# Optimization experiments

Hardware: AMD Instinct MI355X
Metric: run time of the kernel (lower is better)

The kernel has to match this reference:

```python
import jax, jax.numpy as jnp
import numpy as np

B, T, C, H, N = 2, 1024, 2048, 32, 64  # C == H*N, head_size fixed at 64
LAYER, NLAYERS = 12, 24
EPS = 1e-5 * 64.0  # GroupNorm eps = 1e-5 * 8**2


def _structured_params():
    r01 = LAYER / (NLAYERS - 1)          # ratio_0_to_1
    r1a0 = 1.0 - LAYER / NLAYERS         # ratio_1_to_almost0
    ddd = np.arange(C, dtype=np.float64) / C
    n = np.arange(C, dtype=np.float64)
    p = {}
    p['maa_x'] = 1.0 - ddd ** r1a0
    p['maa_w'] = 1.0 - ddd ** r1a0
    p['maa_k'] = 1.0 - ddd ** r1a0
    p['maa_v'] = 1.0 - (ddd ** r1a0 + 0.3 * r01)
    p['maa_r'] = 1.0 - ddd ** (0.5 * r1a0)
    p['maa_g'] = 1.0 - ddd ** (0.5 * r1a0)
    p['time_decay'] = -6.0 + 5.0 * (n / (C - 1)) ** (0.7 + 1.3 * r01)
    zig = ((n + 1) % 3 - 1) * 0.1
    p['u'] = (r01 * (1.0 - n / (C - 1)) + zig).reshape(H, N)  # time_faaaa
    return {k: jnp.asarray(v, jnp.float32) for k, v in p.items()}


def setup_inputs():
    key = jax.random.key(0)
    ks = jax.random.split(key, 12)
    inp = {'x': jax.random.normal(ks[0], (B, T, C), jnp.float32)}
    inp.update(_structured_params())
    inp['maa_w1'] = jax.random.uniform(ks[1], (C, 5 * 32), jnp.float32, -1e-4, 1e-4)
    inp['maa_w2'] = jax.random.uniform(ks[2], (5, 32, C), jnp.float32, -1e-4, 1e-4)
    inp['td_w1'] = jax.random.uniform(ks[3], (C, 64), jnp.float32, -1e-4, 1e-4)
    inp['td_w2'] = jax.random.uniform(ks[4], (64, C), jnp.float32, -1e-4, 1e-4)
    for i, name in enumerate(['Wr', 'Wk', 'Wv', 'Wg', 'Wo']):
        inp[name] = jax.random.normal(ks[5 + i], (C, C), jnp.float32) * 0.02  # applied as x @ W
    inp['ln_g'] = jnp.ones((C,), jnp.float32)
    inp['ln_b'] = jnp.zeros((C,), jnp.float32)
    return inp


def _wkv6(r, k, v, w, u):
    # r,k,v,w: [B,T,C]; u: [H,N].  y_t = r_t . (u*k_t v_t^T + S_t); S_{t+1} = exp(-exp(w_t))*S_t + k_t v_t^T
    def heads(a):
        return a.reshape(B, T, H, N).transpose(1, 0, 2, 3)  # [T,B,H,N]
    r, k, v = heads(r), heads(k), heads(v)
    d = jnp.exp(-jnp.exp(heads(w)))  # data-dependent per-channel decay

    def step(S, inp):
        r_t, k_t, v_t, d_t = inp  # each [B,H,N]
        y = jnp.einsum('bhj,bhji->bhi', r_t, S) \
            + jnp.sum(r_t * u * k_t, axis=-1, keepdims=True) * v_t
        S = d_t[..., None] * S + k_t[..., None] * v_t[..., None, :]
        return S, y

    S0 = jnp.zeros((B, H, N, N), jnp.float32)
    _, y = jax.lax.scan(step, S0, (r, k, v, d))
    return y.transpose(1, 0, 2, 3).reshape(B, T, C)


def reference(x, maa_x, maa_w, maa_k, maa_v, maa_r, maa_g, time_decay, u,
              maa_w1, maa_w2, td_w1, td_w2, Wr, Wk, Wv, Wg, Wo, ln_g, ln_b):
    # token shift: ZeroPad2d((0,0,1,-1)) == shift right by one along T with zero at t=0
    xx = jnp.pad(x, ((0, 0), (1, 0), (0, 0)))[:, :-1] - x
    xxx = x + xx * maa_x
    m = jnp.tanh(xxx @ maa_w1).reshape(B, T, 5, 32)
    m = jnp.einsum('btfd,fdc->fbtc', m, maa_w2)  # [5,B,T,C]
    mw, mk, mv, mr, mg = m[0], m[1], m[2], m[3], m[4]
    xw = x + xx * (maa_w + mw)
    xk = x + xx * (maa_k + mk)
    xv = x + xx * (maa_v + mv)
    xr = x + xx * (maa_r + mr)
    xg = x + xx * (maa_g + mg)
    r = xr @ Wr
    k = xk @ Wk
    v = xv @ Wv
    g = jax.nn.silu(xg @ Wg)
    w = time_decay + jnp.tanh(xw @ td_w1) @ td_w2  # [B,T,C]

    y = _wkv6(r, k, v, w, u)

    # GroupNorm(H groups over C), applied per (b,t) row
    yh = y.reshape(B, T, H, N)
    mu = yh.mean(-1, keepdims=True)
    var = yh.var(-1, keepdims=True)
    yn = (yh - mu) * jax.lax.rsqrt(var + EPS)
    yn = yn * ln_g.reshape(H, N) + ln_b.reshape(H, N)
    y = yn.reshape(B, T, C)
    return (y * g) @ Wo
```

## Files before the change

### kernel.cpp

```cpp
#include <hip/hip_runtime.h>
#include <cstdint>
#include <cstddef>

#define B_  2
#define T_  1024
#define C_  2048
#define H_  32
#define BT_ (B_*T_)
static constexpr float EPS_GN = 1e-5f * 64.0f;

using short8 = __attribute__((ext_vector_type(8))) short;
using f32x4  = __attribute__((ext_vector_type(4))) float;
typedef unsigned short bfu16;

__device__ __forceinline__ bfu16 f2b(float f) {
  uint32_t x = __float_as_uint(f);
  uint32_t r = (x + 0x7FFFu + ((x >> 16) & 1u)) >> 16;
  return (bfu16)r;
}
__device__ __forceinline__ float b2f(bfu16 h) {
  return __uint_as_float(((uint32_t)h) << 16);
}

__device__ __forceinline__ void gload16(const bfu16* g, bfu16* l) {
  __builtin_amdgcn_global_load_lds((__attribute__((address_space(1))) void*)g,
                                   (__attribute__((address_space(3))) void*)l,
                                   16, 0, 0);
}

struct G256P {
  const bfu16* Bt; float* of;
  size_t bStr, oStr;
  int ldk, nkt, kSplit;
  const bfu16* aArr[4];
};

__global__ __launch_bounds__(512, 2)
void gemm256(G256P p)
{
  extern __shared__ __align__(16) bfu16 sm[];
  const int tid  = threadIdx.x;
  const int z    = blockIdx.z;
  const int m0   = blockIdx.y * 256, n0 = blockIdx.x * 256;
  const int lane = tid & 63;
  const int wv   = tid >> 6;
  const int wm   = wv >> 2, wn = wv & 3;
  const int ldk  = p.ldk;

  const bfu16* A;
  size_t koff;
  if (p.kSplit > 1) { A = p.aArr[0]; koff = (size_t)z * p.nkt * 64; }
  else             { A = p.aArr[z]; koff = 0; }
  const bfu16* Bt = p.Bt + (size_t)z * p.bStr;

  const int srow = tid >> 3;
  const int scol = (tid & 7) * 8;
  const int sswz = (srow & 7) << 3;
  const bfu16* gA = A  + (size_t)(m0 + srow) * ldk + koff + (scol ^ sswz);
  const bfu16* gB = Bt + (size_t)(n0 + srow) * ldk + koff + (scol ^ sswz);

  auto STAGE_A = [&](bfu16* dst, int kt) {
    const bfu16* g = gA + (size_t)kt * 64;
    bfu16* l = dst + srow * 64 + scol;
#pragma unroll
    for (int it = 0; it < 4; ++it)
      gload16(g + (size_t)it * 64 * ldk, l + it * 4096);
  };
  auto STAGE_B = [&](bfu16* dst, int kt) {
    const bfu16* g = gB + (size_t)kt * 64;
    bfu16* l = dst + srow * 64 + scol;
#pragma unroll
    for (int it = 0; it < 4; ++it)
      gload16(g + (size_t)it * 64 * ldk, l + it * 4096);
  };

  f32x4 acc[8][4];
  const f32x4 zero = {0.f, 0.f, 0.f, 0.f};
#pragma unroll
  for (int i = 0; i < 8; ++i)
#pragma unroll
    for (int j = 0; j < 4; ++j) acc[i][j] = zero;

  STAGE_A(sm, 0);
  STAGE_B(sm + 32768, 0);

  const int rswz = (lane & 7) << 3;

  for (int kt = 0; kt < p.nkt; ++kt) {
    bfu16* curA = sm + (kt & 1) * 16384;
    bfu16* curB = sm + 32768 + (kt & 1) * 16384;
    bfu16* nxtA = sm + ((kt & 1) ^ 1) * 16384;
    bfu16* nxtB = sm + 32768 + ((kt & 1) ^ 1) * 16384;
    const bool more = (kt + 1 < p.nkt);
    if (more) {
      STAGE_A(nxtA, kt + 1);
      asm volatile("s_waitcnt vmcnt(4)" ::: "memory");
    } else {
      asm volatile("s_waitcnt vmcnt(0)" ::: "memory");
    }
    __builtin_amdgcn_s_barrier();

#pragma unroll
    for (int ks = 0; ks < 2; ++ks) {
      if (ks == 1 && more) STAGE_B(nxtB, kt + 1);
      const int ko = (ks * 32 + (lane >> 4) * 8) ^ rswz;
      short8 a[8], b[4];
#pragma unroll
      for (int i = 0; i < 8; ++i)
        a[i] = *(const short8*)(curA + (wm * 128 + i * 16 + (lane & 15)) * 64 + ko);
#pragma unroll
      for (int j = 0; j < 4; ++j)
        b[j] = *(const short8*)(curB + (wn * 64 + j * 16 + (lane & 15)) * 64 + ko);
      __builtin_amdgcn_s_setprio(1);
#pragma unroll
      for (int i = 0; i < 8; ++i)
#pragma unroll
        for (int j = 0; j < 4; ++j)
          acc[i][j] = __builtin_amdgcn_mfma_f32_16x16x32_bf16(a[i], b[j], acc[i][j], 0, 0, 0);
      __builtin_amdgcn_s_setprio(0);
    }
    __builtin_amdgcn_s_barrier();
  }

  float* o = p.of + (size_t)z * p.oStr;
  const int cb = n0 + wn * 64 + (lane & 15);
  const int rb = m0 + wm * 128 + ((lane >> 4) << 2);
#pragma unroll
  for (int i = 0; i < 8; ++i)
#pragma unroll
    for (int j = 0; j < 4; ++j) {
      int col = cb + j * 16;
#pragma unroll
      for (int q = 0; q < 4; ++q)
        o[(size_t)(rb + i * 16 + q) * 2048 + col] = acc[i][j][q];
    }
}

struct GemmP {
  const bfu16* A; const bfu16* Bt;
  float* of; bfu16* ob;
  const bfu16* xh; const bfu16* xxh;
  int ldk, kIters, kChunk, ldo;
  size_t pStride, aStr, bStr, oStr;
  const float* vArr[5];
};

template<int MODE>
__global__ __launch_bounds__(256)
void gemm_k(GemmP p)
{
  __shared__ alignas(16) bfu16 As[128*64];
  __shared__ alignas(16) bfu16 Bs[128*64];
  const int tid  = threadIdx.x;
  const int z    = blockIdx.z;
  const int m0   = blockIdx.y * 128, n0 = blockIdx.x * 128;
  const int lane = tid & 63;
  const int wv   = tid >> 6;
  const int wr   = (wv >> 1) * 64, wc = (wv & 1) * 64;

  const bfu16* A  = p.A;
  const bfu16* Bt = p.Bt;
  size_t koff = 0;
  if constexpr (MODE == 7) { A += (size_t)z * p.aStr; Bt += (size_t)z * p.bStr; }
  if constexpr (MODE == 5) { koff = (size_t)z * p.kChunk; }

  f32x4 acc[4][4];
  const f32x4 zero = {0.f, 0.f, 0.f, 0.f};
#pragma unroll
  for (int i = 0; i < 4; ++i)
#pragma unroll
    for (int j = 0; j < 4; ++j) acc[i][j] = zero;

  const int srow = tid >> 3;
  const int scol = (tid & 7) * 8;
  const int ldk  = p.ldk;

  for (int kb = 0; kb < p.kIters; ++kb) {
    const bfu16* ga = A  + (size_t)m0 * ldk + koff + kb * 64;
    const bfu16* gb = Bt + (size_t)n0 * ldk + koff + kb * 64;
#pragma unroll
    for (int it = 0; it < 4; ++it) {
      int r = it * 32 + srow;
      gload16(ga + (size_t)r * ldk + scol, As + r * 64 + scol);
      gload16(gb + (size_t)r * ldk + scol, Bs + r * 64 + scol);
    }
    __syncthreads();
#pragma unroll
    for (int kk = 0; kk < 2; ++kk) {
      const int ko = kk * 32 + (lane >> 4) * 8;
      short8 a[4], b[4];
#pragma unroll
      for (int i = 0; i < 4; ++i)
        a[i] = *(const short8*)(As + (wr + i * 16 + (lane & 15)) * 64 + ko);
#pragma unroll
      for (int j = 0; j < 4; ++j)
        b[j] = *(const short8*)(Bs + (wc + j * 16 + (lane & 15)) * 64 + ko);
#pragma unroll
      for (int i = 0; i < 4; ++i)
#pragma unroll
        for (int j = 0; j < 4; ++j)
          acc[i][j] = __builtin_amdgcn_mfma_f32_16x16x32_bf16(a[i], b[j], acc[i][j], 0, 0, 0);
    }
    __syncthreads();
  }

  const int cb = n0 + wc + (lane & 15);
  const int rb = m0 + wr + ((lane >> 4) << 2);
#pragma unroll
  for (int i = 0; i < 4; ++i) {
#pragma unroll
    for (int j = 0; j < 4; ++j) {
      int col = cb + j * 16;
#pragma unroll
      for (int q = 0; q < 4; ++q) {
        int row = rb + i * 16 + q;
        float v = acc[i][j][q];
        if constexpr (MODE == 4) {
          p.of[(size_t)row * p.ldo + col] = p.vArr[0][col] + v;
        } else if constexpr (MODE == 5) {
          p.of[(size_t)z * p.pStride + (size_t)row * p.ldo + col] = v;
        } else if constexpr (MODE == 7) {
          size_t idx = (size_t)row * C_ + col;
          (p.ob + (size_t)z * p.oStr)[idx] =
              f2b(b2f(p.xh[idx]) + b2f(p.xxh[idx]) * (p.vArr[z][col] + v));
        }
      }
    }
  }
}

template<int OUT>
__global__ __launch_bounds__(256)
void redk_tanh(const float* __restrict__ part, size_t pStr, int ldo, int ncols,
               bfu16* __restrict__ out)
{
  int id = blockIdx.x * 256 + threadIdx.x;
  int row = id / ncols, col = id % ncols;
  if (row >= BT_) return;
  float v = 0.f;
#pragma unroll
  for (int s = 0; s < 8; ++s) v += part[(size_t)s * pStr + (size_t)row * ldo + col];
  bfu16 tv = f2b(tanhf(v));
  if constexpr (OUT == 0)
    out[((size_t)(col >> 5) * BT_ + row) * 64 + (col & 31)] = tv;
  else
    out[(size_t)row * 64 + col] = tv;
}

__global__ __launch_bounds__(256)
void redk_sum2(const float* __restrict__ p0, float* __restrict__ out)
{
  size_t i = ((size_t)blockIdx.x * 256 + threadIdx.x) * 4;
  float4 a = *(const float4*)(p0 + i);
  float4 b = *(const float4*)(p0 + (size_t)2048 * 2048 + i);
  a.x += b.x; a.y += b.y; a.z += b.z; a.w += b.w;
  *(float4*)(out + i) = a;
}

struct TrP { const float* src[5]; bfu16* dst; size_t dStr; int R, Cc, Rpad, ldd; };

__global__ __launch_bounds__(256)
void transpose_k(TrP p)
{
  __shared__ float tile[32][33];
  const float* src = p.src[blockIdx.z];
  bfu16* dst = p.dst + (size_t)blockIdx.z * p.dStr;
  const int tx = threadIdx.x & 31, ty = threadIdx.x >> 5;
  const int r0 = blockIdx.y * 32, c0 = blockIdx.x * 32;
#pragma unroll
  for (int i = 0; i < 4; ++i) {
    int r = r0 + ty + i * 8, c = c0 + tx;
    tile[ty + i * 8][tx] = (r < p.R && c < p.Cc) ? src[(size_t)r * p.Cc + c] : 0.f;
  }
  __syncthreads();
#pragma unroll
  for (int i = 0; i < 4; ++i) {
    int c = c0 + ty + i * 8, r = r0 + tx;
    if (c < p.Cc && r < p.Rpad) dst[(size_t)c * p.ldd + r] = f2b(tile[tx][ty + i * 8]);
  }
}

__global__ __launch_bounds__(256)
void prep_xx(const float* __restrict__ x, const float* __restrict__ maa_x,
             bfu16* __restrict__ xxh, bfu16* __restrict__ xxx,
             bfu16* __restrict__ xh)
{
  size_t i = ((size_t)blockIdx.x * 256 + threadIdx.x) * 4;
  int c  = (int)(i & (C_ - 1));
  int bt = (int)(i >> 11);
  int t  = bt & (T_ - 1);
  float4 xv = *(const float4*)(x + i);
  float4 xp = {0.f, 0.f, 0.f, 0.f};
  if (t > 0) xp = *(const float4*)(x + i - C_);
  float4 mx = *(const float4*)(maa_x + c);
  float dx = xp.x - xv.x, dy = xp.y - xv.y, dz = xp.z - xv.z, dw = xp.w - xv.w;
  uint2 w0;
  w0.x = (uint32_t)f2b(dx) | ((uint32_t)f2b(dy) << 16);
  w0.y = (uint32_t)f2b(dz) | ((uint32_t)f2b(dw) << 16);
  *(uint2*)(xxh + i) = w0;
  uint2 w1;
  w1.x = (uint32_t)f2b(xv.x + dx * mx.x) | ((uint32_t)f2b(xv.y + dy * mx.y) << 16);
  w1.y = (uint32_t)f2b(xv.z + dz * mx.z) | ((uint32_t)f2b(xv.w + dw * mx.w) << 16);
  *(uint2*)(xxx + i) = w1;
  uint2 w2;
  w2.x = (uint32_t)f2b(xv.x) | ((uint32_t)f2b(xv.y) << 16);
  w2.y = (uint32_t)f2b(xv.z) | ((uint32_t)f2b(xv.w) << 16);
  *(uint2*)(xh + i) = w2;
}

#define STR 76

__global__ __launch_bounds__(256)
void wkv_a(const float* __restrict__ r, const float* __restrict__ k,
           const float* __restrict__ v, const float* __restrict__ w,
           const float* __restrict__ u, float* __restrict__ rp,
           float* __restrict__ y, float* __restrict__ U, float* __restrict__ G)
{
  __shared__ float rw[64 * STR];
  __shared__ float kk[64 * STR];
  __shared__ float vv[64 * STR];
  __shared__ float Ps[64 * STR];
  __shared__ float red[4][64];
  __shared__ float diag[64];
  __shared__ float Gl[64];

  const int blk = blockIdx.x;
  const int bh = blk >> 4, c = blk & 15;
  const int b = bh >> 5, h = bh & 31;
  const int tid = threadIdx.x;
  const size_t gbase = ((size_t)(b * T_ + c * 64)) * C_ + h * 64;

  {
    const int t = tid >> 2, q = tid & 3;
    const size_t g = gbase + (size_t)t * C_ + q * 16;
    const int l = t * STR + q * 16;
#pragma unroll
    for (int p = 0; p < 4; ++p) {
      *(float4*)(rw + l + p * 4) = *(const float4*)(r + g + p * 4);
      *(float4*)(kk + l + p * 4) = *(const float4*)(k + g + p * 4);
      *(float4*)(vv + l + p * 4) = *(const float4*)(v + g + p * 4);
      float4 wv = *(const float4*)(w + g + p * 4);
      float4 lw;
      lw.x = -__expf(wv.x); lw.y = -__expf(wv.y);
      lw.z = -__expf(wv.z); lw.w = -__expf(wv.w);
      *(float4*)(Ps + l + p * 4) = lw;
    }
  }
  __syncthreads();

  {
    const int seg = tid >> 6, j = tid & 63;
    float loc = 0.f;
#pragma unroll
    for (int tt = 0; tt < 16; ++tt) loc += Ps[(seg * 16 + tt) * STR + j];
    red[seg][j] = loc;
  }
  __syncthreads();
  {
    const int seg = tid >> 6, j = tid & 63;
    float cs = 0.f;
    for (int s = 0; s < seg; ++s) cs += red[s][j];
    const float uj = u[h * 64 + j];
#pragma unroll
    for (int tt = 0; tt < 16; ++tt) {
      const int a = (seg * 16 + tt) * STR + j;
      float lw = Ps[a];
      float rv = rw[a] * __expf(cs);
      rw[a] = rv;
      cs += lw;
      float kv = kk[a] * __expf(-cs);
      kk[a] = kv;
      Ps[a] = rv * kv * uj * __expf(lw);
    }
    if (seg == 3) {
      float Gj = __expf(cs);
      Gl[j] = Gj;
      G[((size_t)bh * 16 + c) * 64 + j] = Gj;
    }
  }
  __syncthreads();

  {
    const int t = tid & 63, q = tid >> 6;
    float s = 0.f;
#pragma unroll
    for (int jj = 0; jj < 16; ++jj) s += Ps[t * STR + q * 16 + jj];
    red[q][t] = s;
  }
  __syncthreads();
  if (tid < 64) diag[tid] = red[0][tid] + red[1][tid] + red[2][tid] + red[3][tid];
  __syncthreads();

  {
    const int tq = tid >> 4, sq = tid & 15;
    float acc[4][4] = {{0.f}};
    if (sq <= tq) {
      for (int j = 0; j < 64; j += 4) {
        float4 a0 = *(const float4*)(rw + (tq * 4 + 0) * STR + j);
        float4 a1 = *(const float4*)(rw + (tq * 4 + 1) * STR + j);
        float4 a2 = *(const float4*)(rw + (tq * 4 + 2) * STR + j);
        float4 a3 = *(const float4*)(rw + (tq * 4 + 3) * STR + j);
        float4 b0 = *(const float4*)(kk + (sq * 4 + 0) * STR + j);
        float4 b1 = *(const float4*)(kk + (sq * 4 + 1) * STR + j);
        float4 b2 = *(const float4*)(kk + (sq * 4 + 2) * STR + j);
        float4 b3 = *(const float4*)(kk + (sq * 4 + 3) * STR + j);
        const float4 av[4] = {a0, a1, a2, a3};
        const float4 bv[4] = {b0, b1, b2, b3};
#pragma unroll
        for (int tt = 0; tt < 4; ++tt)
#pragma unroll
          for (int ss = 0; ss < 4; ++ss)
            acc[tt][ss] += av[tt].x * bv[ss].x + av[tt].y * bv[ss].y
                         + av[tt].z * bv[ss].z + av[tt].w * bv[ss].w;
      }
    }
#pragma unroll
    for (int tt = 0; tt < 4; ++tt)
#pragma unroll
      for (int ss = 0; ss < 4; ++ss) {
        int t = tq * 4 + tt, s = sq * 4 + ss;
        Ps[t * STR + s] = (s < t) ? acc[tt][ss] : (s == t ? diag[t] : 0.f);
      }
  }
  __syncthreads();

  {
    const int tq = tid >> 4, iq = tid & 15;
    float o[4][4] = {{0.f}};
    for (int s4 = 0; s4 <= tq; ++s4) {
#pragma unroll
      for (int ss = 0; ss < 4; ++ss) {
        const int s = s4 * 4 + ss;
        float4 vx = *(const float4*)(vv + s * STR + iq * 4);
        float p0 = Ps[(tq * 4 + 0) * STR + s];
        float p1 = Ps[(tq * 4 + 1) * STR + s];
        float p2 = Ps[(tq * 4 + 2) * STR + s];
        float p3 = Ps[(tq * 4 + 3) * STR + s];
        o[0][0] += p0 * vx.x; o[0][1] += p0 * vx.y; o[0][2] += p0 * vx.z; o[0][3] += p0 * vx.w;
        o[1][0] += p1 * vx.x; o[1][1] += p1 * vx.y; o[1][2] += p1 * vx.z; o[1][3] += p1 * vx.w;
        o[2][0] += p2 * vx.x; o[2][1] += p2 * vx.y; o[2][2] += p2 * vx.z; o[2][3] += p2 * vx.w;
        o[3][0] += p3 * vx.x; o[3][1] += p3 * vx.y; o[3][2] += p3 * vx.z; o[3][3] += p3 * vx.w;
      }
    }
#pragma unroll
    for (int tt = 0; tt < 4; ++tt) {
      float4 ov = {o[tt][0], o[tt][1], o[tt][2], o[tt][3]};
      *(float4*)(y + gbase + (size_t)(tq * 4 + tt) * C_ + iq * 4) = ov;
    }
  }

  {
    const int jq = tid >> 4, iq = tid & 15;
    float ua[4][4] = {{0.f}};
    for (int s = 0; s < 64; ++s) {
      float4 kx = *(const float4*)(kk + s * STR + jq * 4);
      float4 vx = *(const float4*)(vv + s * STR + iq * 4);
      ua[0][0] += kx.x * vx.x; ua[0][1] += kx.x * vx.y; ua[0][2] += kx.x * vx.z; ua[0][3] += kx.x * vx.w;
      ua[1][0] += kx.y * vx.x; ua[1][1] += kx.y * vx.y; ua[1][2] += kx.y * vx.z; ua[1][3] += kx.y * vx.w;
      ua[2][0] += kx.z * vx.x; ua[2][1] += kx.z * vx.y; ua[2][2] += kx.z * vx.z; ua[2][3] += kx.z * vx.w;
      ua[3][0] += kx.w * vx.x; ua[3][1] += kx.w * vx.y; ua[3][2] += kx.w * vx.z; ua[3][3] += kx.w * vx.w;
    }
    const size_t ub = ((size_t)bh * 16 + c) * 4096;
#pragma unroll
    for (int jj = 0; jj < 4; ++jj) {
      float g = Gl[jq * 4 + jj];
      float4 uv = {ua[jj][0] * g, ua[jj][1] * g, ua[jj][2] * g, ua[jj][3] * g};
      *(float4*)(U + ub + (size_t)(jq * 4 + jj) * 64 + iq * 4) = uv;
    }
  }

  {
    const int t = tid >> 2, q = tid & 3;
#pragma unroll
    for (int p = 0; p < 4; ++p)
      *(float4*)(rp + gbase + (size_t)t * C_ + q * 16 + p * 4) =
          *(const float4*)(rw + t * STR + q * 16 + p * 4);
  }
}

__global__ __launch_bounds__(256)
void wkv_b(const float* __restrict__ U, const float* __restrict__ G,
           float* __restrict__ Sbuf)
{
  const int bh = blockIdx.x;
  const int tid = threadIdx.x;
  const int i = tid & 63, jq = tid >> 6;
  __shared__ float Gl[64];
  float S[16];
#pragma unroll
  for (int jj = 0; jj < 16; ++jj) S[jj] = 0.f;
  for (int c = 0; c < 16; ++c) {
    if (tid < 64) Gl[tid] = G[((size_t)bh * 16 + c) * 64 + tid];
    __syncthreads();
    const size_t base = ((size_t)bh * 16 + c) * 4096;
#pragma unroll
    for (int jj = 0; jj < 16; ++jj) {
      const int j = jq * 16 + jj;
      Sbuf[base + (size_t)j * 64 + i] = S[jj];
      S[jj] = Gl[j] * S[jj] + U[base + (size_t)j * 64 + i];
    }
    __syncthreads();
  }
}

__global__ __launch_bounds__(256)
void wkv_c(const float* __restrict__ rp, const float* __restrict__ Sbuf,
           float* __restrict__ y)
{
  __shared__ float Sl[64 * 68];
  __shared__ float rl[64 * 68];
  const int blk = blockIdx.x;
  const int bh = blk >> 4, c = blk & 15;
  const int b = bh >> 5, h = bh & 31;
  const int tid = threadIdx.x;
  const size_t gbase = ((size_t)(b * T_ + c * 64)) * C_ + h * 64;
  {
    const int t = tid >> 2, q = tid & 3;
    const size_t sb = ((size_t)bh * 16 + c) * 4096 + (size_t)t * 64 + q * 16;
    const size_t gr = gbase + (size_t)t * C_ + q * 16;
    const int l = t * 68 + q * 16;
#pragma unroll
    for (int p = 0; p < 4; ++p) {
      *(float4*)(rl + l + p * 4) = *(const float4*)(rp + gr + p * 4);
      *(float4*)(Sl + l + p * 4) = *(const float4*)(Sbuf + sb + p * 4);
    }
  }
  __syncthreads();
  const int tq = tid >> 4, iq = tid & 15;
  float o[4][4] = {{0.f}};
  for (int j = 0; j < 64; ++j) {
    float4 sv = *(const float4*)(Sl + j * 68 + iq * 4);
    float r0 = rl[(tq * 4 + 0) * 68 + j];
    float r1 = rl[(tq * 4 + 1) * 68 + j];
    float r2 = rl[(tq * 4 + 2) * 68 + j];
    float r3 = rl[(tq * 4 + 3) * 68 + j];
    o[0][0] += r0 * sv.x; o[0][1] += r0 * sv.y; o[0][2] += r0 * sv.z; o[0][3] += r0 * sv.w;
    o[1][0] += r1 * sv.x; o[1][1] += r1 * sv.y; o[1][2] += r1 * sv.z; o[1][3] += r1 * sv.w;
    o[2][0] += r2 * sv.x; o[2][1] += r2 * sv.y; o[2][2] += r2 * sv.z; o[2][3] += r2 * sv.w;
    o[3][0] += r3 * sv.x; o[3][1] += r3 * sv.y; o[3][2] += r3 * sv.z; o[3][3] += r3 * sv.w;
  }
#pragma unroll
  for (int tt = 0; tt < 4; ++tt) {
    float* yp = y + gbase + (size_t)(tq * 4 + tt) * C_ + iq * 4;
    float4 yv = *(const float4*)yp;
    yv.x += o[tt][0]; yv.y += o[tt][1]; yv.z += o[tt][2]; yv.w += o[tt][3];
    *(float4*)yp = yv;
  }
}

__global__ __launch_bounds__(256)
void gnorm_kernel(const float* __restrict__ y, const float* __restrict__ gpre,
                  const float* __restrict__ lng, const float* __restrict__ lnb,
                  bfu16* __restrict__ yg)
{
  const int bt = blockIdx.x;
  const int wv = threadIdx.x >> 6, lane = threadIdx.x & 63;
#pragma unroll
  for (int it = 0; it < 8; ++it) {
    int hh = it * 4 + wv;
    int c = hh * 64 + lane;
    size_t idx = (size_t)bt * C_ + c;
    float yv = y[idx];
    float s = yv, sq = yv * yv;
#pragma unroll
    for (int m = 1; m < 64; m <<= 1) {
      s  += __shfl_xor(s, m, 64);
      sq += __shfl_xor(sq, m, 64);
    }
    float mu  = s * (1.f / 64.f);
    float var = sq * (1.f / 64.f) - mu * mu;
    float yn  = (yv - mu) * rsqrtf(var + EPS_GN);
    yn = yn * lng[c] + lnb[c];
    float gp = gpre[idx];
    float gs = gp / (1.f + __expf(-gp));
    yg[idx] = f2b(yn * gs);
  }
}

extern "C" void kernel_launch(void* const* d_in, const int* in_sizes, int n_in,
                              void* d_out, int out_size, void* d_ws, size_t ws_size,
                              hipStream_t stream)
{
  const float* x      = (const float*)d_in[0];
  const float* maa_x  = (const float*)d_in[1];
  const float* maa_w  = (const float*)d_in[2];
  const float* maa_k  = (const float*)d_in[3];
  const float* maa_v  = (const float*)d_in[4];
  const float* maa_r  = (const float*)d_in[5];
  const float* maa_g  = (const float*)d_in[6];
  const float* tdec   = (const float*)d_in[7];
  const float* u      = (const float*)d_in[8];
  const float* maa_w1 = (const float*)d_in[9];
  const float* maa_w2 = (const float*)d_in[10];
  const float* td_w1  = (const float*)d_in[11];
  const float* td_w2  = (const float*)d_in[12];
  const float* lng = (const float*)d_in[18];
  const float* lnb = (const float*)d_in[19];
  float* out = (float*)d_out;

  char* wsp = (char*)d_ws;
  auto alloc = [&](size_t bytes) -> char* {
    char* p = wsp;
    wsp += (bytes + 255) & ~(size_t)255;
    return p;
  };

  bfu16* WT0 = (bfu16*)alloc((size_t)5 * 2048 * 2048 * 2);
  bfu16* w1T  = (bfu16*)alloc((size_t)256 * 2048 * 2);
  bfu16* tw1T = (bfu16*)alloc((size_t)128 * 2048 * 2);
  bfu16* tw2T = (bfu16*)alloc((size_t)2048 * 64 * 2);
  bfu16* w2T  = (bfu16*)alloc((size_t)5 * 2048 * 64 * 2);
  float* ybuf = (float*)alloc((size_t)BT_ * C_ * 4);
  bfu16* xxh  = (bfu16*)alloc((size_t)BT_ * C_ * 2);
  bfu16* xxx  = (bfu16*)alloc((size_t)BT_ * C_ * 2);
  bfu16* xh   = (bfu16*)alloc((size_t)BT_ * C_ * 2);
  bfu16* mtan = (bfu16*)alloc((size_t)5 * BT_ * 64 * 2);
  bfu16* xmix0 = (bfu16*)alloc((size_t)5 * BT_ * C_ * 2);
  float* rbuf = (float*)alloc((size_t)4 * BT_ * C_ * 4);
  float* kbuf = rbuf + (size_t)BT_ * C_;
  float* vbuf = kbuf + (size_t)BT_ * C_;
  float* gbuf = vbuf + (size_t)BT_ * C_;
  float* wbuf = (float*)alloc((size_t)BT_ * C_ * 4);
  bfu16* wtan = (bfu16*)alloc((size_t)BT_ * 64 * 2);
  bfu16* ygb  = xxx;
  float* Ubuf = (float*)(xmix0 + (size_t)1 * BT_ * C_);
  float* Sbuf = (float*)(xmix0 + (size_t)3 * BT_ * C_);
  float* Gbuf = (float*)wtan;
  float* part1 = rbuf;
  float* part3 = wbuf;
  float* partW = rbuf;

  hipMemsetAsync(mtan, 0, (size_t)5 * BT_ * 64 * 2, stream);

  dim3 tb(256);

  {
    TrP p{}; for (int i = 0; i < 5; ++i) p.src[i] = (const float*)d_in[13 + i];
    p.dst = WT0; p.dStr = (size_t)2048 * 2048; p.R = 2048; p.Cc = 2048; p.Rpad = 2048; p.ldd = 2048;
    transpose_k<<<dim3(64, 64, 5), tb, 0, stream>>>(p);
  }
  {
    TrP p{}; p.src[0] = maa_w1; p.dst = w1T; p.dStr = 0;
    p.R = 2048; p.Cc = 160; p.Rpad = 2048; p.ldd = 2048;
    transpose_k<<<dim3(5, 64, 1), tb, 0, stream>>>(p);
  }
  {
    TrP p{}; p.src[0] = td_w1; p.dst = tw1T; p.dStr = 0;
    p.R = 2048; p.Cc = 64; p.Rpad = 2048; p.ldd = 2048;
    transpose_k<<<dim3(2, 64, 1), tb, 0, stream>>>(p);
  }
  {
    TrP p{}; p.src[0] = td_w2; p.dst = tw2T; p.dStr = 0;
    p.R = 64; p.Cc = 2048; p.Rpad = 64; p.ldd = 64;
    transpose_k<<<dim3(64, 2, 1), tb, 0, stream>>>(p);
  }
  {
    TrP p{}; for (int f = 0; f < 5; ++f) p.src[f] = maa_w2 + (size_t)f * 32 * 2048;
    p.dst = w2T; p.dStr = (size_t)2048 * 64;
    p.R = 32; p.Cc = 2048; p.Rpad = 64; p.ldd = 64;
    transpose_k<<<dim3(64, 2, 5), tb, 0, stream>>>(p);
  }

  prep_xx<<<dim3((BT_ * C_ / 4) / 256), tb, 0, stream>>>(x, maa_x, xxh, xxx, xh);

  {
    GemmP p{}; p.A = xxx; p.Bt = w1T; p.ldk = 2048; p.kIters = 4; p.kChunk = 256;
    p.ldo = 256; p.pStride = (size_t)BT_ * 256; p.of = part1;
    gemm_k<5><<<dim3(2, 16, 8), tb, 0, stream>>>(p);
  }
  redk_tanh<0><<<dim3(BT_ * 160 / 256), tb, 0, stream>>>(part1, (size_t)BT_ * 256, 256, 160, mtan);

  {
    GemmP p{}; p.A = mtan; p.Bt = w2T; p.ldk = 64; p.kIters = 1;
    p.aStr = (size_t)BT_ * 64; p.bStr = (size_t)2048 * 64; p.oStr = (size_t)BT_ * C_;
    p.ob = xmix0; p.xh = xh; p.xxh = xxh;
    p.vArr[0] = maa_w; p.vArr[1] = maa_k; p.vArr[2] = maa_v; p.vArr[3] = maa_r; p.vArr[4] = maa_g;
    gemm_k<7><<<dim3(16, 16, 5), tb, 0, stream>>>(p);
  }

  {
    G256P p{}; p.Bt = WT0; p.ldk = 2048; p.nkt = 32; p.kSplit = 1;
    p.bStr = (size_t)2048 * 2048; p.oStr = (size_t)BT_ * C_; p.of = rbuf;
    p.aArr[0] = xmix0 + (size_t)3 * BT_ * C_;
    p.aArr[1] = xmix0 + (size_t)1 * BT_ * C_;
    p.aArr[2] = xmix0 + (size_t)2 * BT_ * C_;
    p.aArr[3] = xmix0 + (size_t)4 * BT_ * C_;
    gemm256<<<dim3(8, 8, 4), dim3(512), 131072, stream>>>(p);
  }

  {
    GemmP p{}; p.A = xmix0; p.Bt = tw1T; p.ldk = 2048; p.kIters = 4; p.kChunk = 256;
    p.ldo = 128; p.pStride = (size_t)BT_ * 128; p.of = part3;
    gemm_k<5><<<dim3(1, 16, 8), tb, 0, stream>>>(p);
  }
  redk_tanh<1><<<dim3(BT_ * 64 / 256), tb, 0, stream>>>(part3, (size_t)BT_ * 128, 128, 64, wtan);

  {
    GemmP p{}; p.A = wtan; p.Bt = tw2T; p.ldk = 64; p.kIters = 1;
    p.of = wbuf; p.ldo = 2048; p.vArr[0] = tdec;
    gemm_k<4><<<dim3(16, 16, 1), tb, 0, stream>>>(p);
  }

  wkv_a<<<dim3(1024), tb, 0, stream>>>(rbuf, kbuf, vbuf, wbuf, u, rbuf, ybuf, Ubuf, Gbuf);
  wkv_b<<<dim3(64),   tb, 0, stream>>>(Ubuf, Gbuf, Sbuf);
  wkv_c<<<dim3(1024), tb, 0, stream>>>(rbuf, Sbuf, ybuf);

  gnorm_kernel<<<dim3(BT_), tb, 0, stream>>>(ybuf, gbuf, lng, lnb, ygb);

  {
    G256P p{}; p.Bt = WT0 + (size_t)4 * 2048 * 2048; p.ldk = 2048;
    p.nkt = 16; p.kSplit = 2;
    p.bStr = 0; p.oStr = (size_t)2048 * 2048; p.of = partW;
    p.aArr[0] = ygb;
    gemm256<<<dim3(8, 8, 2), dim3(512), 131072, stream>>>(p);
  }
  redk_sum2<<<dim3(4096), tb, 0, stream>>>(partW, out);
}
```

Baseline: 340.6 us.

## Deepen gemm256 prefetch pipeline, split K four ways, fuse decay exp into GEMM

Restructures the 256x256 GEMM main loop to prefetch combined A/B tiles two k-steps ahead, reading all LDS fragments before a barrier and then issuing the next load ahead of the MFMAs. The output projection now uses a 4-way K split to fill more CUs, reduced by a 4-input sum kernel. The -exp(w) decay transform moves into the td_w2 GEMM epilogue instead of the WKV loader. The cost is more partial-sum traffic and a larger partial buffer, which must hold four slices.

```diff
diff --git a/kernel.cpp b/kernel.cpp
--- a/kernel.cpp
+++ b/kernel.cpp
@@ -46,11 +46,12 @@
   const int wv   = tid >> 6;
   const int wm   = wv >> 2, wn = wv & 3;
   const int ldk  = p.ldk;
+  const int nkt  = p.nkt;
 
   const bfu16* A;
   size_t koff;
-  if (p.kSplit > 1) { A = p.aArr[0]; koff = (size_t)z * p.nkt * 64; }
-  else             { A = p.aArr[z]; koff = 0; }
+  if (p.kSplit > 1) { A = p.aArr[0]; koff = (size_t)z * nkt * 64; }
+  else              { A = p.aArr[z]; koff = 0; }
   const bfu16* Bt = p.Bt + (size_t)z * p.bStr;
 
   const int srow = tid >> 3;
@@ -59,19 +60,16 @@
   const bfu16* gA = A  + (size_t)(m0 + srow) * ldk + koff + (scol ^ sswz);
   const bfu16* gB = Bt + (size_t)(n0 + srow) * ldk + koff + (scol ^ sswz);
 
-  auto STAGE_A = [&](bfu16* dst, int kt) {
-    const bfu16* g = gA + (size_t)kt * 64;
-    bfu16* l = dst + srow * 64 + scol;
-#pragma unroll
-    for (int it = 0; it < 4; ++it)
-      gload16(g + (size_t)it * 64 * ldk, l + it * 4096);
-  };
-  auto STAGE_B = [&](bfu16* dst, int kt) {
-    const bfu16* g = gB + (size_t)kt * 64;
-    bfu16* l = dst + srow * 64 + scol;
-#pragma unroll
-    for (int it = 0; it < 4; ++it)
-      gload16(g + (size_t)it * 64 * ldk, l + it * 4096);
+  auto STAGE = [&](int t) {
+    bfu16* la = sm + (t & 1) * 32768 + srow * 64 + scol;
+    bfu16* lb = la + 16384;
+    const bfu16* ga = gA + (size_t)t * 64;
+    const bfu16* gb = gB + (size_t)t * 64;
+#pragma unroll
+    for (int it = 0; it < 4; ++it) {
+      gload16(ga + (size_t)it * 64 * ldk, la + it * 4096);
+      gload16(gb + (size_t)it * 64 * ldk, lb + it * 4096);
+    }
   };
 
   f32x4 acc[8][4];
@@ -81,45 +79,47 @@
 #pragma unroll
     for (int j = 0; j < 4; ++j) acc[i][j] = zero;
 
-  STAGE_A(sm, 0);
-  STAGE_B(sm + 32768, 0);
+  STAGE(0);
+  STAGE(1);
 
   const int rswz = (lane & 7) << 3;
-
-  for (int kt = 0; kt < p.nkt; ++kt) {
-    bfu16* curA = sm + (kt & 1) * 16384;
-    bfu16* curB = sm + 32768 + (kt & 1) * 16384;
-    bfu16* nxtA = sm + ((kt & 1) ^ 1) * 16384;
-    bfu16* nxtB = sm + 32768 + ((kt & 1) ^ 1) * 16384;
-    const bool more = (kt + 1 < p.nkt);
-    if (more) {
-      STAGE_A(nxtA, kt + 1);
-      asm volatile("s_waitcnt vmcnt(4)" ::: "memory");
-    } else {
-      asm volatile("s_waitcnt vmcnt(0)" ::: "memory");
-    }
+  const int arow = wm * 128 + (lane & 15);
+  const int brow = wn * 64 + (lane & 15);
+  const int kbase = (lane >> 4) * 8;
+
+  for (int kt = 0; kt < nkt; ++kt) {
+    if (kt + 1 < nkt) { asm volatile("s_waitcnt vmcnt(8)" ::: "memory"); }
+    else              { asm volatile("s_waitcnt vmcnt(0)" ::: "memory"); }
     __builtin_amdgcn_s_barrier();
 
+    const bfu16* curA = sm + (kt & 1) * 32768;
+    const bfu16* curB = curA + 16384;
+    short8 a[8][2], b[4][2];
 #pragma unroll
     for (int ks = 0; ks < 2; ++ks) {
-      if (ks == 1 && more) STAGE_B(nxtB, kt + 1);
-      const int ko = (ks * 32 + (lane >> 4) * 8) ^ rswz;
-      short8 a[8], b[4];
+      const int ko = (ks * 32 + kbase) ^ rswz;
+#pragma unroll
+      for (int j = 0; j < 4; ++j)
+        b[j][ks] = *(const short8*)(curB + (brow + j * 16) * 64 + ko);
 #pragma unroll
       for (int i = 0; i < 8; ++i)
-        a[i] = *(const short8*)(curA + (wm * 128 + i * 16 + (lane & 15)) * 64 + ko);
-#pragma unroll
-      for (int j = 0; j < 4; ++j)
-        b[j] = *(const short8*)(curB + (wn * 64 + j * 16 + (lane & 15)) * 64 + ko);
-      __builtin_amdgcn_s_setprio(1);
+        a[i][ks] = *(const short8*)(curA + (arow + i * 16) * 64 + ko);
+    }
+    asm volatile("s_waitcnt lgkmcnt(0)" ::: "memory");
+    __builtin_amdgcn_sched_barrier(0);
+    __builtin_amdgcn_s_barrier();
+    if (kt + 2 < nkt) STAGE(kt + 2);
+    __builtin_amdgcn_sched_barrier(0);
+
+    __builtin_amdgcn_s_setprio(1);
+#pragma unroll
+    for (int ks = 0; ks < 2; ++ks)
 #pragma unroll
       for (int i = 0; i < 8; ++i)
 #pragma unroll
         for (int j = 0; j < 4; ++j)
-          acc[i][j] = __builtin_amdgcn_mfma_f32_16x16x32_bf16(a[i], b[j], acc[i][j], 0, 0, 0);
-      __builtin_amdgcn_s_setprio(0);
-    }
-    __builtin_amdgcn_s_barrier();
+          acc[i][j] = __builtin_amdgcn_mfma_f32_16x16x32_bf16(a[i][ks], b[j][ks], acc[i][j], 0, 0, 0);
+    __builtin_amdgcn_s_setprio(0);
   }
 
   float* o = p.of + (size_t)z * p.oStr;
@@ -216,7 +216,7 @@
         int row = rb + i * 16 + q;
         float v = acc[i][j][q];
         if constexpr (MODE == 4) {
-          p.of[(size_t)row * p.ldo + col] = p.vArr[0][col] + v;
+          p.of[(size_t)row * p.ldo + col] = -__expf(p.vArr[0][col] + v);
         } else if constexpr (MODE == 5) {
           p.of[(size_t)z * p.pStride + (size_t)row * p.ldo + col] = v;
         } else if constexpr (MODE == 7) {
@@ -248,12 +248,16 @@
 }
 
 __global__ __launch_bounds__(256)
-void redk_sum2(const float* __restrict__ p0, float* __restrict__ out)
+void redk_sum4(const float* __restrict__ p0, float* __restrict__ out)
 {
   size_t i = ((size_t)blockIdx.x * 256 + threadIdx.x) * 4;
+  const size_t str = (size_t)2048 * 2048;
   float4 a = *(const float4*)(p0 + i);
-  float4 b = *(const float4*)(p0 + (size_t)2048 * 2048 + i);
-  a.x += b.x; a.y += b.y; a.z += b.z; a.w += b.w;
+  float4 b = *(const float4*)(p0 + str + i);
+  float4 c = *(const float4*)(p0 + 2 * str + i);
+  float4 d = *(const float4*)(p0 + 3 * str + i);
+  a.x += b.x + c.x + d.x; a.y += b.y + c.y + d.y;
+  a.z += b.z + c.z + d.z; a.w += b.w + c.w + d.w;
   *(float4*)(out + i) = a;
 }
 
@@ -339,11 +343,7 @@
       *(float4*)(rw + l + p * 4) = *(const float4*)(r + g + p * 4);
       *(float4*)(kk + l + p * 4) = *(const float4*)(k + g + p * 4);
       *(float4*)(vv + l + p * 4) = *(const float4*)(v + g + p * 4);
-      float4 wv = *(const float4*)(w + g + p * 4);
-      float4 lw;
-      lw.x = -__expf(wv.x); lw.y = -__expf(wv.y);
-      lw.z = -__expf(wv.z); lw.w = -__expf(wv.w);
-      *(float4*)(Ps + l + p * 4) = lw;
+      *(float4*)(Ps + l + p * 4) = *(const float4*)(w + g + p * 4);
     }
   }
   __syncthreads();
@@ -709,10 +709,10 @@
 
   {
     G256P p{}; p.Bt = WT0 + (size_t)4 * 2048 * 2048; p.ldk = 2048;
-    p.nkt = 16; p.kSplit = 2;
+    p.nkt = 8; p.kSplit = 4;
     p.bStr = 0; p.oStr = (size_t)2048 * 2048; p.of = partW;
     p.aArr[0] = ygb;
-    gemm256<<<dim3(8, 8, 2), dim3(512), 131072, stream>>>(p);
-  }
-  redk_sum2<<<dim3(4096), tb, 0, stream>>>(partW, out);
-}
+    gemm256<<<dim3(8, 8, 4), dim3(512), 131072, stream>>>(p);
+  }
+  redk_sum4<<<dim3(4096), tb, 0, stream>>>(partW, out);
+}
```

Measured after the change: 345.6 us. No clear change (+1.5%).
